# Kernel tuning notes

Measured on AMD Instinct MI355X. Metric: run time of the kernel, lower is better.

The kernel has to match this reference:

```python
import jax, jax.numpy as jnp
import numpy as np

N_NODES = 100000
N_EDGES = 3200000
IN_C, HID_C, OUT_C = 128, 64, 64


def setup_inputs() -> dict:
    key = jax.random.key(0)
    k = jax.random.split(key, 6)
    x = jax.random.normal(k[0], (N_NODES, IN_C), dtype=jnp.float32)
    edge_index = jax.random.randint(k[1], (2, N_EDGES), 0, N_NODES, dtype=jnp.int64)
    edge_weight = jax.random.uniform(k[2], (N_EDGES,), dtype=jnp.float32)
    W1 = jax.random.normal(k[3], (IN_C, HID_C), dtype=jnp.float32) * (1.0 / np.sqrt(IN_C))
    b1 = jnp.zeros((HID_C,), dtype=jnp.float32)
    W2 = jax.random.normal(k[4], (HID_C, OUT_C), dtype=jnp.float32) * (1.0 / np.sqrt(HID_C))
    b2 = jnp.zeros((OUT_C,), dtype=jnp.float32)
    return {"x": x, "edge_index": edge_index, "edge_weight": edge_weight,
            "W1": W1, "b1": b1, "W2": W2, "b2": b2}


def _gcn_norm(edge_index, edge_weight, num_nodes, dtype):
    # PyG GCNConv default: add self-loops (weight 1), symmetric normalization
    loop = jnp.arange(num_nodes, dtype=edge_index.dtype)
    row = jnp.concatenate([edge_index[0], loop])  # sources
    col = jnp.concatenate([edge_index[1], loop])  # targets (aggregation dim)
    w = jnp.concatenate([edge_weight.astype(dtype), jnp.ones((num_nodes,), dtype)])
    deg = jax.ops.segment_sum(w, col, num_segments=num_nodes)
    deg_inv_sqrt = jnp.where(deg > 0, jax.lax.rsqrt(deg), jnp.zeros((), dtype))
    norm = deg_inv_sqrt[row] * w * deg_inv_sqrt[col]
    return row, col, norm


def _gcn_conv(h, row, col, norm, W, b, num_nodes):
    h = h @ W                      # [N, C_out]
    msg = h[row] * norm[:, None]   # gather over sources, scale by edge norm
    out = jax.ops.segment_sum(msg, col, num_segments=num_nodes)  # scatter-add to targets
    return out + b


def reference(x, edge_index, edge_weight, W1, b1, W2, b2):
    num_nodes = x.shape[0]
    row, col, norm = _gcn_norm(edge_index, edge_weight, num_nodes, x.dtype)
    h = _gcn_conv(x, row, col, norm, W1, b1, num_nodes)
    h = jax.nn.relu(h)
    return _gcn_conv(h, row, col, norm, W2, b2, num_nodes)
```

## Files before the change

kernel.cpp:

```cpp
#include <hip/hip_runtime.h>
#include <hip/hip_bf16.h>

#define N_NODES 100000
#define N_EDGES 3200000
#define IN_C 128
#define HID_C 64
#define OUT_C 64

#define NBUCKET 196
#define SC_EDGES 4096
#define SC_PER   (SC_EDGES / 256)
#define SC_GRID  782
#define CAP 18432
#define MM1_GRID (N_NODES / 16)

struct EdgeRec { int s; float v; };

typedef float f32x2 __attribute__((ext_vector_type(2)));
typedef float f32x4 __attribute__((ext_vector_type(4)));
typedef short bf16x8 __attribute__((ext_vector_type(8)));
union F8 { uint4 u; bf16x8 f; };

__device__ __forceinline__ unsigned pack_bf16(float lo, float hi) {
    unsigned short l = __hip_bfloat16_raw(__float2bfloat16(lo)).x;
    unsigned short h = __hip_bfloat16_raw(__float2bfloat16(hi)).x;
    return ((unsigned)h << 16) | l;
}
__device__ __forceinline__ float bf_lo(unsigned u) {
    union { unsigned u; float f; } c; c.u = u << 16; return c.f;
}
__device__ __forceinline__ float bf_hi(unsigned u) {
    union { unsigned u; float f; } c; c.u = u & 0xffff0000u; return c.f;
}
__device__ __forceinline__ f32x2 bfp(unsigned u) {
    union { unsigned u; float f; } lo, hi;
    lo.u = u << 16; hi.u = u & 0xffff0000u;
    f32x2 r; r.x = lo.f; r.y = hi.f; return r;
}
__device__ __forceinline__ void pk_fma(f32x2& acc, f32x2 a, f32x2 w) {
    asm("v_pk_fma_f32 %0, %1, %2, %0" : "+v"(acc) : "v"(a), "v"(w));
}
__device__ __forceinline__ void edge_acc(f32x2* acc2, uint4 u, float w) {
    f32x2 wv; wv.x = w; wv.y = w;
    pk_fma(acc2[0], bfp(u.x), wv);
    pk_fma(acc2[1], bfp(u.y), wv);
    pk_fma(acc2[2], bfp(u.z), wv);
    pk_fma(acc2[3], bfp(u.w), wv);
}
__device__ __forceinline__ unsigned cvt_pk_bf16(float lo, float hi) {
    unsigned r;
    asm("v_cvt_pk_bf16_f32 %0, %1, %2" : "=v"(r) : "v"(lo), "v"(hi));
    return r;
}
__device__ __forceinline__ void split_frag(const float* f, uint4& hi4, uint4& lo4) {
    unsigned hi[4], lo[4];
    #pragma unroll
    for (int p = 0; p < 4; ++p) {
        hi[p] = cvt_pk_bf16(f[2 * p], f[2 * p + 1]);
        float r0 = f[2 * p]     - bf_lo(hi[p]);
        float r1 = f[2 * p + 1] - bf_hi(hi[p]);
        lo[p] = cvt_pk_bf16(r0, r1);
    }
    hi4 = make_uint4(hi[0], hi[1], hi[2], hi[3]);
    lo4 = make_uint4(lo[0], lo[1], lo[2], lo[3]);
}

__device__ __forceinline__ void scatter_body(const int* __restrict__ ei,
                                             const float* __restrict__ ew,
                                             int* __restrict__ gcursor,
                                             uint2* __restrict__ tmp,
                                             int* hist, int* scn, int* lcur,
                                             int* adj, uint2* rec,
                                             unsigned char* bk) {
    int tid = threadIdx.x;
    hist[tid] = 0;
    __syncthreads();
    int base = blockIdx.x * SC_EDGES;
    unsigned ys[SC_PER];
    float    ws[SC_PER];
    int      bs[SC_PER];
    for (int i = 0; i < SC_PER; ++i) {
        int e = base + i * 256 + tid;
        if (e < N_EDGES) {
            int t = ei[N_EDGES + e];
            bs[i] = t >> 9;
            ys[i] = (unsigned)ei[e] | ((unsigned)(t & 511) << 17);
            ws[i] = ew[e];
            atomicAdd(&hist[bs[i]], 1);
        } else bs[i] = -1;
    }
    __syncthreads();
    int v = hist[tid];
    scn[tid] = v;
    __syncthreads();
    for (int off = 1; off < 256; off <<= 1) {
        int t = scn[tid];
        int add = (tid >= off) ? scn[tid - off] : 0;
        __syncthreads();
        scn[tid] = t + add;
        __syncthreads();
    }
    int excl = scn[tid] - v;
    int gb = (v > 0) ? atomicAdd(&gcursor[tid], v) : 0;
    lcur[tid] = excl;
    adj[tid] = tid * CAP + gb - excl;
    __syncthreads();
    for (int i = 0; i < SC_PER; ++i) {
        if (bs[i] >= 0) {
            int j = atomicAdd(&lcur[bs[i]], 1);
            rec[j] = make_uint2(__float_as_uint(ws[i]), ys[i]);
            bk[j] = (unsigned char)bs[i];
        }
    }
    __syncthreads();
    int count = N_EDGES - base;
    if (count > SC_EDGES) count = SC_EDGES;
    for (int j = tid; j < count; j += 256) {
        int b = bk[j];
        tmp[adj[b] + j] = rec[j];
    }
}

template<int K>
__device__ __forceinline__ void mm_tile_bf(int tile,
                                           const float* __restrict__ X,
                                           const F8* bhi, const F8* blo,
                                           int lr, int kr, int col,
                                           unsigned* __restrict__ h) {
    constexpr int NKS = K / 32;
    int row0 = tile * 16;
    const float* xbase = X + (size_t)(row0 + lr) * K + kr * 8;
    float4 xa[NKS], xb[NKS];
    #pragma unroll
    for (int ks = 0; ks < NKS; ++ks) {
        const float4* xp = (const float4*)(xbase + ks * 32);
        xa[ks] = xp[0];
        xb[ks] = xp[1];
    }
    f32x4 acc = {0.f, 0.f, 0.f, 0.f};
    #pragma unroll
    for (int ks = 0; ks < NKS; ++ks) {
        float f[8] = {xa[ks].x, xa[ks].y, xa[ks].z, xa[ks].w,
                      xb[ks].x, xb[ks].y, xb[ks].z, xb[ks].w};
        F8 ahi, alo;
        split_frag(f, ahi.u, alo.u);
        acc = __builtin_amdgcn_mfma_f32_16x16x32_bf16(ahi.f, bhi[ks].f, acc, 0, 0, 0);
        acc = __builtin_amdgcn_mfma_f32_16x16x32_bf16(ahi.f, blo[ks].f, acc, 0, 0, 0);
        acc = __builtin_amdgcn_mfma_f32_16x16x32_bf16(alo.f, bhi[ks].f, acc, 0, 0, 0);
    }
    int rbase = row0 + kr * 4;
    float v0 = acc[0], v1 = acc[1], v2 = acc[2], v3 = acc[3];
    float o0 = __shfl_xor(v0, 1, 64);
    float o1 = __shfl_xor(v1, 1, 64);
    float o2 = __shfl_xor(v2, 1, 64);
    float o3 = __shfl_xor(v3, 1, 64);
    if ((lr & 1) == 0) {
        int ci = col >> 1;
        h[(rbase + 0) * 32 + ci] = pack_bf16(v0, o0);
        h[(rbase + 1) * 32 + ci] = pack_bf16(v1, o1);
        h[(rbase + 2) * 32 + ci] = pack_bf16(v2, o2);
        h[(rbase + 3) * 32 + ci] = pack_bf16(v3, o3);
    }
}

template<int K>
__device__ __forceinline__ void load_bfrags(const float* __restrict__ W,
                                            int kr, int col, F8* bhi, F8* blo) {
    #pragma unroll
    for (int ks = 0; ks < K / 32; ++ks) {
        const float* wp = W + (ks * 32 + kr * 8) * 64 + col;
        float f[8];
        #pragma unroll
        for (int j = 0; j < 8; ++j) f[j] = wp[j * 64];
        split_frag(f, bhi[ks].u, blo[ks].u);
    }
}

__global__ __launch_bounds__(256) void fused_scatter_mm1(const int* __restrict__ ei,
                                                         const float* __restrict__ ew,
                                                         int* __restrict__ gcursor,
                                                         uint2* __restrict__ tmp,
                                                         const float* __restrict__ x,
                                                         const float* __restrict__ W1,
                                                         unsigned* __restrict__ h) {
    __shared__ int hist[256];
    __shared__ int scn[256];
    __shared__ int lcur[256];
    __shared__ int adj[256];
    __shared__ uint2 rec[SC_EDGES];
    __shared__ unsigned char bk[SC_EDGES];
    if (blockIdx.x >= SC_GRID) {
        int l  = threadIdx.x & 63;
        int lr = l & 15;
        int kr = l >> 4;
        int col = (threadIdx.x >> 6) * 16 + lr;
        F8 bhi[IN_C / 32], blo[IN_C / 32];
        load_bfrags<IN_C>(W1, kr, col, bhi, blo);
        mm_tile_bf<IN_C>(blockIdx.x - SC_GRID, x, bhi, blo, lr, kr, col, h);
        return;
    }
    scatter_body(ei, ew, gcursor, tmp, hist, scn, lcur, adj, rec, bk);
}

template<int K>
__global__ __launch_bounds__(256) void mm_mfma_raw(const float* __restrict__ X,
                                                   const float* __restrict__ W,
                                                   unsigned* __restrict__ h) {
    int l  = threadIdx.x & 63;
    int lr = l & 15;
    int kr = l >> 4;
    int col = (threadIdx.x >> 6) * 16 + lr;
    F8 bhi[K / 32], blo[K / 32];
    load_bfrags<K>(W, kr, col, bhi, blo);
    for (int t = blockIdx.x; t < N_NODES / 16; t += gridDim.x)
        mm_tile_bf<K>(t, X, bhi, blo, lr, kr, col, h);
}

__global__ __launch_bounds__(256) void bucket_scan(const int* __restrict__ gcnt,
                                                   int* __restrict__ start) {
    __shared__ int s[256];
    int tid = threadIdx.x;
    int v = gcnt[tid];
    s[tid] = v;
    __syncthreads();
    for (int off = 1; off < 256; off <<= 1) {
        int t = s[tid];
        int add = (tid >= off) ? s[tid - off] : 0;
        __syncthreads();
        s[tid] = t + add;
        __syncthreads();
    }
    start[tid] = s[tid] - v;
    if (tid == 255) start[256] = s[255];
}

__global__ __launch_bounds__(512) void fine_count(const int* __restrict__ start,
                                                  const uint2* __restrict__ tmpPad,
                                                  int* __restrict__ rowptr,
                                                  float* __restrict__ dis) {
    __shared__ int   cnt[512];
    __shared__ float wdeg[512];
    __shared__ int   s[512];
    int tid = threadIdx.x;
    int nodeBase = blockIdx.x << 9;
    int bb = start[blockIdx.x];
    int nEdge = start[blockIdx.x + 1] - bb;
    const uint2* tb = tmpPad + (size_t)blockIdx.x * CAP;
    cnt[tid] = 0;
    wdeg[tid] = 0.f;
    __syncthreads();
    for (int e = tid; e < nEdge; e += 512) {
        uint2 r = tb[e];
        int l = (r.y >> 17) & 511;
        atomicAdd(&cnt[l], 1);
        atomicAdd(&wdeg[l], __uint_as_float(r.x));
    }
    __syncthreads();
    int v = cnt[tid];
    s[tid] = v;
    __syncthreads();
    for (int off = 1; off < 512; off <<= 1) {
        int t = s[tid];
        int add = (tid >= off) ? s[tid - off] : 0;
        __syncthreads();
        s[tid] = t + add;
        __syncthreads();
    }
    int excl = s[tid] - v;
    int node = nodeBase + tid;
    if (node < N_NODES) {
        rowptr[node] = bb + excl;
        dis[node] = rsqrtf(wdeg[tid] + 1.0f);
    }
    if (node == N_NODES) rowptr[N_NODES] = N_EDGES;
}

__global__ __launch_bounds__(512) void fine_place(const int* __restrict__ start,
                                                  const uint2* __restrict__ tmpPad,
                                                  const int* __restrict__ rowptr,
                                                  const float* __restrict__ dis,
                                                  EdgeRec* __restrict__ ed) {
    __shared__ int cnt[512];
    int tid = threadIdx.x;
    int nodeBase = blockIdx.x << 9;
    int bb = start[blockIdx.x];
    int nEdge = start[blockIdx.x + 1] - bb;
    const uint2* tb = tmpPad + (size_t)blockIdx.x * CAP;
    int node = nodeBase + tid;
    cnt[tid] = ((node < N_NODES) ? rowptr[node] : N_EDGES) - bb;
    __syncthreads();
    for (int e = tid; e < nEdge; e += 512) {
        uint2 r = tb[e];
        int l = (r.y >> 17) & 511;
        int src = (int)(r.y & 0x1FFFFu);
        int p = atomicAdd(&cnt[l], 1);
        EdgeRec o;
        o.s = src;
        o.v = __uint_as_float(r.x) * dis[src];
        ed[bb + p] = o;
    }
}

__global__ __launch_bounds__(256, 8) void agg_kernel(const int* __restrict__ rowptr,
                                                     const EdgeRec* __restrict__ ed,
                                                     const unsigned* __restrict__ h,
                                                     const float* __restrict__ dis,
                                                     const float* __restrict__ b,
                                                     float* __restrict__ out,
                                                     int relu) {
    int node = blockIdx.x * 4 + (threadIdx.x >> 6);
    int lane = threadIdx.x & 63;
    int g = lane >> 3;
    int cl = lane & 7;
    int beg = rowptr[node];
    int end = rowptr[node + 1];
    const uint4* h16 = (const uint4*)h;
    const char*  hb  = (const char*)h + (size_t)cl * 16;
    float d  = dis[node];
    uint4 us = h16[(size_t)node * 8 + cl];
    f32x2 acc2[4];
    acc2[0] = 0.f; acc2[1] = 0.f; acc2[2] = 0.f; acc2[3] = 0.f;
    int n = end - beg;
    int nb = (n + 31) >> 5;
    int nm1 = n - 1;
    uint2 q0, q1, q2, q3;
    if (nb > 0) {
        q0 = *(const uint2*)(ed + beg + min(g,      nm1));
        q1 = *(const uint2*)(ed + beg + min(g + 8,  nm1));
        q2 = *(const uint2*)(ed + beg + min(g + 16, nm1));
        q3 = *(const uint2*)(ed + beg + min(g + 24, nm1));
        for (int bt = 0; bt < nb; ++bt) {
            int ob = (bt << 5) + g;
            float w0 = (ob      < n) ? __uint_as_float(q0.y) : 0.f;
            float w1 = (ob + 8  < n) ? __uint_as_float(q1.y) : 0.f;
            float w2 = (ob + 16 < n) ? __uint_as_float(q2.y) : 0.f;
            float w3 = (ob + 24 < n) ? __uint_as_float(q3.y) : 0.f;
            uint4 u0 = *(const uint4*)(hb + ((size_t)(unsigned)q0.x << 7));
            uint4 u1 = *(const uint4*)(hb + ((size_t)(unsigned)q1.x << 7));
            uint4 u2 = *(const uint4*)(hb + ((size_t)(unsigned)q2.x << 7));
            uint4 u3 = *(const uint4*)(hb + ((size_t)(unsigned)q3.x << 7));
            if (bt + 1 < nb) {
                int on = ob + 32;
                q0 = *(const uint2*)(ed + beg + min(on,      nm1));
                q1 = *(const uint2*)(ed + beg + min(on + 8,  nm1));
                q2 = *(const uint2*)(ed + beg + min(on + 16, nm1));
                q3 = *(const uint2*)(ed + beg + min(on + 24, nm1));
            }
            edge_acc(acc2, u0, w0);
            edge_acc(acc2, u1, w1);
            edge_acc(acc2, u2, w2);
            edge_acc(acc2, u3, w3);
        }
    }
    float acc[8] = { acc2[0].x, acc2[0].y, acc2[1].x, acc2[1].y,
                     acc2[2].x, acc2[2].y, acc2[3].x, acc2[3].y };
    #pragma unroll
    for (int kk = 0; kk < 8; ++kk) {
        acc[kk] += __shfl_xor(acc[kk], 8, 64);
        acc[kk] += __shfl_xor(acc[kk], 16, 64);
        acc[kk] += __shfl_xor(acc[kk], 32, 64);
    }
    if (g == 0) {
        float hs[8] = { bf_lo(us.x), bf_hi(us.x), bf_lo(us.y), bf_hi(us.y),
                        bf_lo(us.z), bf_hi(us.z), bf_lo(us.w), bf_hi(us.w) };
        const float4* b4 = (const float4*)b;
        float4 bv0 = b4[cl * 2], bv1 = b4[cl * 2 + 1];
        float4 v0, v1;
        v0.x = d * (acc[0] + d * hs[0]) + bv0.x;
        v0.y = d * (acc[1] + d * hs[1]) + bv0.y;
        v0.z = d * (acc[2] + d * hs[2]) + bv0.z;
        v0.w = d * (acc[3] + d * hs[3]) + bv0.w;
        v1.x = d * (acc[4] + d * hs[4]) + bv1.x;
        v1.y = d * (acc[5] + d * hs[5]) + bv1.y;
        v1.z = d * (acc[6] + d * hs[6]) + bv1.z;
        v1.w = d * (acc[7] + d * hs[7]) + bv1.w;
        if (relu) {
            v0.x = fmaxf(v0.x, 0.f); v0.y = fmaxf(v0.y, 0.f);
            v0.z = fmaxf(v0.z, 0.f); v0.w = fmaxf(v0.w, 0.f);
            v1.x = fmaxf(v1.x, 0.f); v1.y = fmaxf(v1.y, 0.f);
            v1.z = fmaxf(v1.z, 0.f); v1.w = fmaxf(v1.w, 0.f);
        }
        float4* o4 = (float4*)out;
        o4[node * 16 + cl * 2]     = v0;
        o4[node * 16 + cl * 2 + 1] = v1;
    }
}

extern "C" void kernel_launch(void* const* d_in, const int* in_sizes, int n_in,
                              void* d_out, int out_size, void* d_ws, size_t ws_size,
                              hipStream_t stream) {
    const float* x  = (const float*)d_in[0];
    const int*   ei = (const int*)d_in[1];
    const float* ew = (const float*)d_in[2];
    const float* W1 = (const float*)d_in[3];
    const float* b1 = (const float*)d_in[4];
    const float* W2 = (const float*)d_in[5];
    const float* b2 = (const float*)d_in[6];
    float* out = (float*)d_out;

    char* p = (char*)d_ws;
    auto carve = [&](size_t bytes) { char* r = p; p += (bytes + 255) & ~(size_t)255; return r; };
    int*      rowptr  = (int*)carve((N_NODES + 1) * 4);
    int*      start   = (int*)carve(257 * 4);
    int*      gcursor = (int*)carve(256 * 4);
    float*    dis     = (float*)carve(N_NODES * 4);
    EdgeRec*  ed      = (EdgeRec*)carve((size_t)N_EDGES * 8);
    unsigned* h       = (unsigned*)carve((size_t)N_NODES * 64 * 2);
    size_t    tmpsz   = (size_t)NBUCKET * CAP * 8;
    size_t    asz     = (size_t)N_NODES * 64 * 4;
    char*     r2      = carve(tmpsz > asz ? tmpsz : asz);
    uint2*    tmpPad  = (uint2*)r2;
    float*    a       = (float*)r2;

    hipMemsetAsync(gcursor, 0, 256 * sizeof(int), stream);

    fused_scatter_mm1<<<SC_GRID + MM1_GRID, 256, 0, stream>>>(ei, ew, gcursor,
                                                              tmpPad, x, W1, h);
    bucket_scan<<<1, 256, 0, stream>>>(gcursor, start);
    fine_count<<<NBUCKET, 512, 0, stream>>>(start, tmpPad, rowptr, dis);
    fine_place<<<NBUCKET, 512, 0, stream>>>(start, tmpPad, rowptr, dis, ed);

    agg_kernel<<<N_NODES / 4, 256, 0, stream>>>(rowptr, ed, h, dis, b1, a, 1);

    mm_mfma_raw<HID_C><<<1250, 256, 0, stream>>>(a, W2, h);
    agg_kernel<<<N_NODES / 4, 256, 0, stream>>>(rowptr, ed, h, dis, b2, out, 0);
}
```

Baseline: 357.2 us.

## Fuse bucket scan, fine count and fine place into one sort kernel

Merges the single-block bucket prefix scan, the per-bucket count and the placement kernel into one fine_sort kernel. Each block redoes the 256-entry scan redundantly, and the placement pass reuses the in-register exclusive offsets, so two launches and a rowptr reread go away. Because dis for other buckets is not ready inside the fused kernel, the source-side dis factor moves into agg_kernel as an extra gather per edge. That adds a random 4-byte read per edge in both aggregation passes.

```diff
diff --git a/kernel.cpp b/kernel.cpp
--- a/kernel.cpp
+++ b/kernel.cpp
@@ -216,36 +216,30 @@
         mm_tile_bf<K>(t, X, bhi, blo, lr, kr, col, h);
 }
 
-__global__ __launch_bounds__(256) void bucket_scan(const int* __restrict__ gcnt,
-                                                   int* __restrict__ start) {
-    __shared__ int s[256];
-    int tid = threadIdx.x;
-    int v = gcnt[tid];
-    s[tid] = v;
-    __syncthreads();
-    for (int off = 1; off < 256; off <<= 1) {
-        int t = s[tid];
-        int add = (tid >= off) ? s[tid - off] : 0;
-        __syncthreads();
-        s[tid] = t + add;
-        __syncthreads();
-    }
-    start[tid] = s[tid] - v;
-    if (tid == 255) start[256] = s[255];
-}
-
-__global__ __launch_bounds__(512) void fine_count(const int* __restrict__ start,
-                                                  const uint2* __restrict__ tmpPad,
-                                                  int* __restrict__ rowptr,
-                                                  float* __restrict__ dis) {
+__global__ __launch_bounds__(512) void fine_sort(const int* __restrict__ gcursor,
+                                                 const uint2* __restrict__ tmpPad,
+                                                 int* __restrict__ rowptr,
+                                                 float* __restrict__ dis,
+                                                 EdgeRec* __restrict__ ed) {
     __shared__ int   cnt[512];
     __shared__ float wdeg[512];
     __shared__ int   s[512];
+    __shared__ int   bsc[256];
     int tid = threadIdx.x;
-    int nodeBase = blockIdx.x << 9;
-    int bb = start[blockIdx.x];
-    int nEdge = start[blockIdx.x + 1] - bb;
-    const uint2* tb = tmpPad + (size_t)blockIdx.x * CAP;
+    if (tid < 256) bsc[tid] = gcursor[tid];
+    __syncthreads();
+    for (int off = 1; off < 256; off <<= 1) {
+        int t = (tid < 256) ? bsc[tid] : 0;
+        int add = (tid < 256 && tid >= off) ? bsc[tid - off] : 0;
+        __syncthreads();
+        if (tid < 256) bsc[tid] = t + add;
+        __syncthreads();
+    }
+    int bkt = blockIdx.x;
+    int nEdge = gcursor[bkt];
+    int bb = bsc[bkt] - nEdge;
+    int nodeBase = bkt << 9;
+    const uint2* tb = tmpPad + (size_t)bkt * CAP;
     cnt[tid] = 0;
     wdeg[tid] = 0.f;
     __syncthreads();
@@ -273,30 +267,15 @@
         dis[node] = rsqrtf(wdeg[tid] + 1.0f);
     }
     if (node == N_NODES) rowptr[N_NODES] = N_EDGES;
-}
-
-__global__ __launch_bounds__(512) void fine_place(const int* __restrict__ start,
-                                                  const uint2* __restrict__ tmpPad,
-                                                  const int* __restrict__ rowptr,
-                                                  const float* __restrict__ dis,
-                                                  EdgeRec* __restrict__ ed) {
-    __shared__ int cnt[512];
-    int tid = threadIdx.x;
-    int nodeBase = blockIdx.x << 9;
-    int bb = start[blockIdx.x];
-    int nEdge = start[blockIdx.x + 1] - bb;
-    const uint2* tb = tmpPad + (size_t)blockIdx.x * CAP;
-    int node = nodeBase + tid;
-    cnt[tid] = ((node < N_NODES) ? rowptr[node] : N_EDGES) - bb;
+    cnt[tid] = excl;
     __syncthreads();
     for (int e = tid; e < nEdge; e += 512) {
         uint2 r = tb[e];
         int l = (r.y >> 17) & 511;
-        int src = (int)(r.y & 0x1FFFFu);
         int p = atomicAdd(&cnt[l], 1);
         EdgeRec o;
-        o.s = src;
-        o.v = __uint_as_float(r.x) * dis[src];
+        o.s = (int)(r.y & 0x1FFFFu);
+        o.v = __uint_as_float(r.x);
         ed[bb + p] = o;
     }
 }
@@ -331,10 +310,10 @@
         q3 = *(const uint2*)(ed + beg + min(g + 24, nm1));
         for (int bt = 0; bt < nb; ++bt) {
             int ob = (bt << 5) + g;
-            float w0 = (ob      < n) ? __uint_as_float(q0.y) : 0.f;
-            float w1 = (ob + 8  < n) ? __uint_as_float(q1.y) : 0.f;
-            float w2 = (ob + 16 < n) ? __uint_as_float(q2.y) : 0.f;
-            float w3 = (ob + 24 < n) ? __uint_as_float(q3.y) : 0.f;
+            float w0 = (ob      < n) ? __uint_as_float(q0.y) * dis[(int)q0.x] : 0.f;
+            float w1 = (ob + 8  < n) ? __uint_as_float(q1.y) * dis[(int)q1.x] : 0.f;
+            float w2 = (ob + 16 < n) ? __uint_as_float(q2.y) * dis[(int)q2.x] : 0.f;
+            float w3 = (ob + 24 < n) ? __uint_as_float(q3.y) * dis[(int)q3.x] : 0.f;
             uint4 u0 = *(const uint4*)(hb + ((size_t)(unsigned)q0.x << 7));
             uint4 u1 = *(const uint4*)(hb + ((size_t)(unsigned)q1.x << 7));
             uint4 u2 = *(const uint4*)(hb + ((size_t)(unsigned)q2.x << 7));
@@ -401,7 +380,6 @@
     char* p = (char*)d_ws;
     auto carve = [&](size_t bytes) { char* r = p; p += (bytes + 255) & ~(size_t)255; return r; };
     int*      rowptr  = (int*)carve((N_NODES + 1) * 4);
-    int*      start   = (int*)carve(257 * 4);
     int*      gcursor = (int*)carve(256 * 4);
     float*    dis     = (float*)carve(N_NODES * 4);
     EdgeRec*  ed      = (EdgeRec*)carve((size_t)N_EDGES * 8);
@@ -416,9 +394,7 @@
 
     fused_scatter_mm1<<<SC_GRID + MM1_GRID, 256, 0, stream>>>(ei, ew, gcursor,
                                                               tmpPad, x, W1, h);
-    bucket_scan<<<1, 256, 0, stream>>>(gcursor, start);
-    fine_count<<<NBUCKET, 512, 0, stream>>>(start, tmpPad, rowptr, dis);
-    fine_place<<<NBUCKET, 512, 0, stream>>>(start, tmpPad, rowptr, dis, ed);
+    fine_sort<<<NBUCKET, 512, 0, stream>>>(gcursor, tmpPad, rowptr, dis, ed);
 
     agg_kernel<<<N_NODES / 4, 256, 0, stream>>>(rowptr, ed, h, dis, b1, a, 1);
 
```

Result: slower. 398.5 us (+11.5%).
